# Kernel tuning notes

Hardware: AMD Instinct MI355X
Metric: run time of the kernel (lower is better)

Reference implementation:

```python
import jax, jax.numpy as jnp
import numpy as np

N, E, IN, H, B, R, ND, K, ER = 50000, 800000, 256, 256, 256, 8, 5000, 16, 20000
LAM = 0.7


def _gat(x, src, dst, W, a_src, a_dst, b):
    """Single-head PyG-style GATConv, add_self_loops=False."""
    h = x @ W                                   # [N,H]
    s = (h @ a_src)[src] + (h @ a_dst)[dst]     # [E]
    e = jax.nn.leaky_relu(s, 0.2)
    m = jax.ops.segment_max(e, dst, num_segments=N)
    m = jnp.where(jnp.isneginf(m), 0.0, m)
    p = jnp.exp(e - m[dst])
    z = jax.ops.segment_sum(p, dst, num_segments=N)
    alpha = p / (z[dst] + 1e-16)                # softmax over incoming edges
    out = jax.ops.segment_sum(alpha[:, None] * h[src], dst, num_segments=N)
    return out + b


def setup_inputs() -> dict:
    key = jax.random.key(0)
    ks = jax.random.split(key, 20)
    d = {}
    d['x'] = jax.random.normal(ks[0], (N, IN), dtype=jnp.float32)
    d['edge_index'] = jax.random.randint(ks[1], (2, E), 0, N)
    d['head_indices'] = jax.random.randint(ks[2], (B,), 0, N)
    d['rel_types'] = jax.random.randint(ks[3], (B,), 0, R)
    d['tail_indices'] = jax.random.randint(ks[4], (B,), 0, N)
    d['g2l'] = jax.random.randint(ks[5], (N,), 0, ND)
    d['rel_edge_src'] = jax.random.randint(ks[6], (3, ER), 0, ND)
    d['sim_neighbors'] = jax.random.randint(ks[7], (ND, K), 0, N)
    d['sim_weights'] = jax.random.uniform(ks[8], (ND, K), dtype=jnp.float32) / K
    sc1 = 1.0 / np.sqrt(IN)
    sc2 = 1.0 / np.sqrt(H)
    d['W1'] = jax.random.normal(ks[9], (IN, H), dtype=jnp.float32) * sc1
    d['a1_src'] = jax.random.normal(ks[10], (H,), dtype=jnp.float32) * sc2
    d['a1_dst'] = jax.random.normal(ks[11], (H,), dtype=jnp.float32) * sc2
    d['b1'] = jnp.zeros((H,), dtype=jnp.float32)
    d['W2'] = jax.random.normal(ks[12], (H, H), dtype=jnp.float32) * sc2
    d['a2_src'] = jax.random.normal(ks[13], (H,), dtype=jnp.float32) * sc2
    d['a2_dst'] = jax.random.normal(ks[14], (H,), dtype=jnp.float32) * sc2
    d['b2'] = jnp.zeros((H,), dtype=jnp.float32)
    d['rel_emb'] = jax.random.normal(ks[15], (R, H), dtype=jnp.float32) * sc2
    return d


def reference(x, edge_index, head_indices, rel_types, tail_indices, g2l,
              rel_edge_src, sim_neighbors, sim_weights,
              W1, a1_src, a1_dst, b1, W2, a2_src, a2_dst, b2, rel_emb):
    src, dst = edge_index[0], edge_index[1]
    # Encoder: GAT -> SiLU -> GAT
    h = _gat(x, src, dst, W1, a1_src, a1_dst, b1)
    h = jax.nn.silu(h)
    node_emb = _gat(h, src, dst, W2, a2_src, a2_dst, b2)  # [N,H]

    # Sequential per-triplet disease-embedding modification (rel 4/5/6)
    def step(emb, tr):
        hi, r = tr
        is_dis = (r >= 4) & (r <= 6)
        ridx = jnp.clip(r - 4, 0, 2)
        local = g2l[hi]
        deg = jnp.sum(rel_edge_src[ridx] == local).astype(emb.dtype)
        c = LAM * jnp.exp(-LAM * deg) + 0.2
        nb = sim_neighbors[local]           # [K]
        w = sim_weights[local]              # [K]
        vec = (w[:, None] * emb[nb]).sum(0)  # weighted neighbor mix
        new = c * vec + (1.0 - c) * emb[hi]
        row = jnp.where(is_dis, new, emb[hi])
        return emb.at[hi].set(row), None

    node_emb, _ = jax.lax.scan(step, node_emb, (head_indices, rel_types))

    # DistMult decode
    head = node_emb[head_indices]
    tail = node_emb[tail_indices]
    rel = rel_emb[rel_types]
    score = (head * rel * tail).sum(-1)
    return jax.nn.sigmoid(score)
```

## Files before the change

### kernel.cpp

```cpp
#include <hip/hip_runtime.h>
#include <cstdint>

#define N_NODES 50000
#define N_EDGES 800000
#define DIM     256
#define BSZ     256
#define ND_     5000
#define KNB     16
#define ER_     20000
#define LAM     0.7f

typedef unsigned int uint;
typedef unsigned short ushort;
typedef __attribute__((ext_vector_type(8))) short bf16x8;
typedef __attribute__((ext_vector_type(4))) float f32x4;

#define MTILES_PAD 3128
#define M_PAD      (MTILES_PAD*16)
#define NB_SCAN    ((N_NODES + 255) / 256)

__device__ __forceinline__ ushort f2bf(float f) {
    uint u = __float_as_uint(f);
    uint r = u + 0x7FFFu + ((u >> 16) & 1u);
    return (ushort)(r >> 16);
}
__device__ __forceinline__ float bflo(uint u) { return __uint_as_float(u << 16); }
__device__ __forceinline__ float bfhi(uint u) { return __uint_as_float(u & 0xffff0000u); }


__global__ __launch_bounds__(256)
void pack_a_kernel(const float* __restrict__ A, ushort* __restrict__ out, int M) {
    const int mt = blockIdx.x;
    const int t  = threadIdx.x;
    const int l  = t & 63;
    const int kt0 = (t >> 6) * 2;
    const int row = mt * 16 + (l & 15);
    const int lg  = l >> 4;
#pragma unroll
    for (int p = 0; p < 2; ++p) {
        int kt = kt0 + p;
        float4 v0 = make_float4(0.f, 0.f, 0.f, 0.f);
        float4 v1 = make_float4(0.f, 0.f, 0.f, 0.f);
        if (row < M) {
            v0 = *(const float4*)(A + (size_t)row * 256 + kt * 32 + lg * 4);
            v1 = *(const float4*)(A + (size_t)row * 256 + kt * 32 + lg * 4 + 16);
        }
        ushort us[8];
        us[0] = f2bf(v0.x); us[1] = f2bf(v0.y); us[2] = f2bf(v0.z); us[3] = f2bf(v0.w);
        us[4] = f2bf(v1.x); us[5] = f2bf(v1.y); us[6] = f2bf(v1.z); us[7] = f2bf(v1.w);
        ushort* dst = out + ((size_t)(mt * 8 + kt) * 64 + l) * 8;
        *(uint4*)dst = *(uint4*)us;
    }
}

__global__ __launch_bounds__(256)
void pack_a_bf16_kernel(const ushort* __restrict__ A, ushort* __restrict__ out, int M) {
    const int mt = blockIdx.x;
    const int t  = threadIdx.x;
    const int l  = t & 63;
    const int kt0 = (t >> 6) * 2;
    const int row = mt * 16 + (l & 15);
    const int lg  = l >> 4;
#pragma unroll
    for (int p = 0; p < 2; ++p) {
        int kt = kt0 + p;
        uint2 v0 = make_uint2(0u, 0u), v1 = make_uint2(0u, 0u);
        if (row < M) {
            v0 = *(const uint2*)(A + (size_t)row * 256 + kt * 32 + lg * 4);
            v1 = *(const uint2*)(A + (size_t)row * 256 + kt * 32 + 16 + lg * 4);
        }
        uint4 o; o.x = v0.x; o.y = v0.y; o.z = v1.x; o.w = v1.y;
        *(uint4*)(out + ((size_t)(mt * 8 + kt) * 64 + l) * 8) = o;
    }
}

__global__ __launch_bounds__(256)
void pack_b_kernel(const float* __restrict__ W, ushort* __restrict__ out) {
    const int nt = blockIdx.x;
    const int t  = threadIdx.x;
    const int l  = t & 63;
    const int kt0 = (t >> 6) * 2;
    const int n  = nt * 16 + (l & 15);
    const int lg = l >> 4;
#pragma unroll
    for (int p = 0; p < 2; ++p) {
        int kt = kt0 + p;
        ushort us[8];
#pragma unroll
        for (int j = 0; j < 8; ++j) {
            int kk = (j & 3) + lg * 4 + (j >> 2) * 16;
            us[j] = f2bf(W[(size_t)(kt * 32 + kk) * 256 + n]);
        }
        ushort* dst = out + ((size_t)(nt * 8 + kt) * 64 + l) * 8;
        *(uint4*)dst = *(uint4*)us;
    }
}

__global__ __launch_bounds__(256)
void gemm_bf16_kernel(const ushort* __restrict__ Ap, const ushort* __restrict__ Bp,
                      ushort* __restrict__ H,
                      const float* __restrict__ a_src, const float* __restrict__ a_dst,
                      float* __restrict__ hs, float* __restrict__ hd, int M) {
    __shared__ float sdS[4][64];
    __shared__ float sdD[4][64];
    const int t = threadIdx.x;
    const int w = t >> 6;
    const int l = t & 63;
    const int mt0 = blockIdx.x * 4;
    f32x4 acc[4][4];
#pragma unroll
    for (int i = 0; i < 4; ++i)
#pragma unroll
        for (int j = 0; j < 4; ++j) acc[i][j] = (f32x4){0.f, 0.f, 0.f, 0.f};

    for (int kt = 0; kt < 8; ++kt) {
        bf16x8 af[4], bfr[4];
#pragma unroll
        for (int mi = 0; mi < 4; ++mi)
            af[mi] = *(const bf16x8*)(Ap + ((size_t)((mt0 + mi) * 8 + kt) * 64 + l) * 8);
#pragma unroll
        for (int ni = 0; ni < 4; ++ni)
            bfr[ni] = *(const bf16x8*)(Bp + ((size_t)((w * 4 + ni) * 8 + kt) * 64 + l) * 8);
#pragma unroll
        for (int mi = 0; mi < 4; ++mi)
#pragma unroll
            for (int ni = 0; ni < 4; ++ni)
                acc[mi][ni] = __builtin_amdgcn_mfma_f32_16x16x32_bf16(
                    af[mi], bfr[ni], acc[mi][ni], 0, 0, 0);
    }
    const int rbase = (l >> 4) * 4;
    const int cb    = (l & 15);
    float asv[4], adv[4];
#pragma unroll
    for (int ni = 0; ni < 4; ++ni) {
        int col = (w * 4 + ni) * 16 + cb;
        asv[ni] = a_src[col];
        adv[ni] = a_dst[col];
    }
#pragma unroll
    for (int mi = 0; mi < 4; ++mi) {
#pragma unroll
        for (int r = 0; r < 4; ++r) {
            int row = (mt0 + mi) * 16 + rbase + r;
            float ps = 0.f, pd = 0.f;
#pragma unroll
            for (int ni = 0; ni < 4; ++ni) {
                float hv = acc[mi][ni][r];
                ps = fmaf(hv, asv[ni], ps);
                pd = fmaf(hv, adv[ni], pd);
                if (row < M) {
                    int col = (w * 4 + ni) * 16 + cb;
                    H[(size_t)row * 256 + col] = f2bf(hv);
                }
            }
#pragma unroll
            for (int o = 1; o < 16; o <<= 1) {
                ps += __shfl_xor(ps, o);
                pd += __shfl_xor(pd, o);
            }
            if (cb == 0) {
                sdS[w][mi * 16 + rbase + r] = ps;
                sdD[w][mi * 16 + rbase + r] = pd;
            }
        }
    }
    __syncthreads();
    if (t < 64) {
        int row = mt0 * 16 + t;
        if (row < M) {
            hs[row] = sdS[0][t] + sdS[1][t] + sdS[2][t] + sdS[3][t];
            hd[row] = sdD[0][t] + sdD[1][t] + sdD[2][t] + sdD[3][t];
        }
    }
}

__global__ __launch_bounds__(256)
void hist_kernel(const int* __restrict__ ei, int* __restrict__ deg) {
    int e = blockIdx.x * 256 + threadIdx.x;
    if (e < N_EDGES) atomicAdd(&deg[ei[N_EDGES + e]], 1);
}

__global__ __launch_bounds__(256)
void blockscan_kernel(const int* __restrict__ deg, int* __restrict__ off,
                      int* __restrict__ bsum) {
    __shared__ int s[256];
    const int b = blockIdx.x, t = threadIdx.x;
    const int idx = b * 256 + t;
    int v = (idx < N_NODES) ? deg[idx] : 0;
    s[t] = v;
    __syncthreads();
    for (int o = 1; o < 256; o <<= 1) {
        int x = (t >= o) ? s[t - o] : 0;
        __syncthreads();
        s[t] += x;
        __syncthreads();
    }
    if (idx < N_NODES) off[idx] = s[t] - v;
    if (t == 255) bsum[b] = s[255];
}

__global__ __launch_bounds__(256)
void scan_bsum_kernel(const int* __restrict__ bsum, int* __restrict__ bpre) {
    __shared__ int s[256];
    const int t = threadIdx.x;
    int v = (t < NB_SCAN) ? bsum[t] : 0;
    s[t] = v;
    __syncthreads();
    for (int o = 1; o < 256; o <<= 1) {
        int x = (t >= o) ? s[t - o] : 0;
        __syncthreads();
        s[t] += x;
        __syncthreads();
    }
    if (t < NB_SCAN) bpre[t] = s[t] - v;
    if (t == 255) bpre[NB_SCAN] = s[255];
}

__global__ __launch_bounds__(256)
void add_offsets_kernel(int* __restrict__ off, const int* __restrict__ bpre) {
    const int b = blockIdx.x, t = threadIdx.x;
    const int idx = b * 256 + t;
    if (idx < N_NODES) off[idx] += bpre[b];
    if (b == NB_SCAN - 1 && t == 255) off[N_NODES] = bpre[NB_SCAN];
}

__global__ __launch_bounds__(256)
void scatter_kernel(const int* __restrict__ ei, const int* __restrict__ off,
                    int* __restrict__ cnt, int* __restrict__ csr_src) {
    int e = blockIdx.x * 256 + threadIdx.x;
    if (e >= N_EDGES) return;
    int d = ei[N_EDGES + e];
    int pos = atomicAdd(&cnt[d], 1);
    csr_src[off[d] + pos] = ei[e];
}

__global__ __launch_bounds__(256)
void gat_aggr_kernel(const int* __restrict__ off, const int* __restrict__ csr_src,
                     const float* __restrict__ hs, const float* __restrict__ hd,
                     const ushort* __restrict__ hb, const float* __restrict__ bias,
                     float* __restrict__ out_f32, ushort* __restrict__ out_bf,
                     int do_silu) {
    const int d = blockIdx.x * 4 + (threadIdx.x >> 6);
    const int l = threadIdx.x & 63;
    if (d >= N_NODES) return;
    const int beg = off[d], end = off[d + 1];
    const float hdd = hd[d];

    float acc0 = 0.f, acc1 = 0.f, acc2 = 0.f, acc3 = 0.f;
    float zl = 0.f;
    const ushort* __restrict__ hcol = hb + l * 4;

    for (int c0 = beg; c0 < end; c0 += 64) {
        const int cn = min(end - c0, 64);
        int s = 0; float pexp = 0.f;
        if (l < cn) {
            s = csr_src[c0 + l];
            float v = hs[s] + hdd;
            v = (v >= 0.f) ? v : 0.2f * v;
            pexp = __expf(v);
        }
        zl += pexp;
        int j = 0;
        for (; j + 4 <= cn; j += 4) {
            int   s0 = __shfl(s, j),     s1 = __shfl(s, j + 1);
            int   s2 = __shfl(s, j + 2), s3 = __shfl(s, j + 3);
            float p0 = __shfl(pexp, j),     p1 = __shfl(pexp, j + 1);
            float p2 = __shfl(pexp, j + 2), p3 = __shfl(pexp, j + 3);
            uint2 r0 = *(const uint2*)(hcol + (size_t)s0 * DIM);
            uint2 r1 = *(const uint2*)(hcol + (size_t)s1 * DIM);
            uint2 r2 = *(const uint2*)(hcol + (size_t)s2 * DIM);
            uint2 r3 = *(const uint2*)(hcol + (size_t)s3 * DIM);
            acc0 = fmaf(p0, bflo(r0.x), acc0); acc1 = fmaf(p0, bfhi(r0.x), acc1);
            acc2 = fmaf(p0, bflo(r0.y), acc2); acc3 = fmaf(p0, bfhi(r0.y), acc3);
            acc0 = fmaf(p1, bflo(r1.x), acc0); acc1 = fmaf(p1, bfhi(r1.x), acc1);
            acc2 = fmaf(p1, bflo(r1.y), acc2); acc3 = fmaf(p1, bfhi(r1.y), acc3);
            acc0 = fmaf(p2, bflo(r2.x), acc0); acc1 = fmaf(p2, bfhi(r2.x), acc1);
            acc2 = fmaf(p2, bflo(r2.y), acc2); acc3 = fmaf(p2, bfhi(r2.y), acc3);
            acc0 = fmaf(p3, bflo(r3.x), acc0); acc1 = fmaf(p3, bfhi(r3.x), acc1);
            acc2 = fmaf(p3, bflo(r3.y), acc2); acc3 = fmaf(p3, bfhi(r3.y), acc3);
        }
        for (; j < cn; ++j) {
            int   sj = __shfl(s, j);
            float pj = __shfl(pexp, j);
            uint2 rv = *(const uint2*)(hcol + (size_t)sj * DIM);
            acc0 = fmaf(pj, bflo(rv.x), acc0); acc1 = fmaf(pj, bfhi(rv.x), acc1);
            acc2 = fmaf(pj, bflo(rv.y), acc2); acc3 = fmaf(pj, bfhi(rv.y), acc3);
        }
    }
    float z = zl;
#pragma unroll
    for (int o = 32; o; o >>= 1) z += __shfl_xor(z, o);
    const float inv = (end > beg) ? 1.f / (z + 1e-16f) : 0.f;
    float4 bb = *(const float4*)(bias + l * 4);
    float o0 = acc0 * inv + bb.x;
    float o1 = acc1 * inv + bb.y;
    float o2 = acc2 * inv + bb.z;
    float o3 = acc3 * inv + bb.w;
    if (do_silu) {
        o0 = o0 / (1.f + __expf(-o0));
        o1 = o1 / (1.f + __expf(-o1));
        o2 = o2 / (1.f + __expf(-o2));
        o3 = o3 / (1.f + __expf(-o3));
    }
    if (out_bf) {
        ushort us[4] = {f2bf(o0), f2bf(o1), f2bf(o2), f2bf(o3)};
        *(uint2*)(out_bf + (size_t)d * DIM + l * 4) = *(uint2*)us;
    } else {
        *(float4*)(out_f32 + (size_t)d * DIM + l * 4) = make_float4(o0, o1, o2, o3);
    }
}

__global__ __launch_bounds__(256)
void rel_hist_kernel(const int* __restrict__ res, int* __restrict__ rhist) {
    int i = blockIdx.x * 256 + threadIdx.x;
    if (i < 3 * ER_) atomicAdd(&rhist[(i / ER_) * ND_ + res[i]], 1);
}

__global__ __launch_bounds__(256)
void cvals_kernel(const int* __restrict__ rel, const int* __restrict__ head,
                  const int* __restrict__ g2l, const int* __restrict__ rhist,
                  float* __restrict__ cvals) {
    int b = threadIdx.x;
    int r = rel[b];
    float c = 0.f;
    if (r >= 4 && r <= 6) {
        int local = g2l[head[b]];
        int deg = rhist[(r - 4) * ND_ + local];
        c = LAM * __expf(-LAM * (float)deg) + 0.2f;
    }
    cvals[b] = c;
}

__global__ __launch_bounds__(256)
void prep_steps_kernel(const float* __restrict__ emb, const int* __restrict__ head,
                       const int* __restrict__ rel, const int* __restrict__ g2l,
                       const int* __restrict__ nbs, const float* __restrict__ wts,
                       float* __restrict__ vecpre, int* __restrict__ W,
                       int* __restrict__ flags) {
    int b = blockIdx.x;
    int t = threadIdx.x;
    int r = rel[b];
    int dis = (r >= 4 && r <= 6);
    if (t == 0) { flags[b] = 0; W[b] = dis ? head[b] : -1; }
    if (!dis) return;
    int local = g2l[head[b]];
    const int* __restrict__ nb = nbs + (size_t)local * KNB;
    const float* __restrict__ w = wts + (size_t)local * KNB;
    float v0 = 0.f, v1 = 0.f;
#pragma unroll
    for (int k = 0; k < KNB; k += 2) {
        v0 = fmaf(w[k],     emb[(size_t)nb[k] * DIM + t],     v0);
        v1 = fmaf(w[k + 1], emb[(size_t)nb[k + 1] * DIM + t], v1);
    }
    vecpre[(size_t)b * DIM + t] = v0 + v1;
}

__global__ __launch_bounds__(256)
void conflict_kernel(const int* __restrict__ W, const int* __restrict__ head,
                     const int* __restrict__ rel, const int* __restrict__ g2l,
                     const int* __restrict__ nbs, int* __restrict__ flags) {
    int b = blockIdx.x;
    int r = rel[b];
    if (r < 4 || r > 6) return;
    __shared__ int rd[KNB + 1];
    int t = threadIdx.x;
    if (t == 0) rd[KNB] = head[b];
    if (t < KNB) {
        int local = g2l[head[b]];
        rd[t] = nbs[(size_t)local * KNB + t];
    }
    __syncthreads();
    int w = (t != b) ? W[t] : -1;
    if (w >= 0) {
        bool hit = false;
#pragma unroll
        for (int k = 0; k <= KNB; ++k) hit |= (rd[k] == w);
        if (hit) { flags[b] = 1; flags[t] = 1; }
    }
}

__global__ __launch_bounds__(256)
void apply_par_kernel(float* __restrict__ emb, const int* __restrict__ head,
                      const int* __restrict__ rel, const float* __restrict__ cvals,
                      const float* __restrict__ vecpre, const int* __restrict__ flags) {
    int b = blockIdx.x;
    int r = rel[b];
    if (r < 4 || r > 6) return;
    if (flags[b]) return;
    int t = threadIdx.x;
    int hi = head[b];
    float c = cvals[b];
    size_t idx = (size_t)hi * DIM + t;
    emb[idx] = c * vecpre[(size_t)b * DIM + t] + (1.f - c) * emb[idx];
}

__global__ __launch_bounds__(256)
void apply_seq_kernel(float* __restrict__ emb, const int* __restrict__ head,
                      const int* __restrict__ rel, const int* __restrict__ g2l,
                      const int* __restrict__ nbs, const float* __restrict__ wts,
                      const float* __restrict__ cvals, const int* __restrict__ flags) {
    __shared__ int   snb[BSZ][KNB];
    __shared__ float sw[BSZ][KNB];
    __shared__ int   sh[BSZ];
    __shared__ float sc[BSZ];
    __shared__ int   sf[BSZ];
    const int t = threadIdx.x;
    int r = rel[t];
    int dis = (r >= 4 && r <= 6);
    int hi = head[t];
    sh[t] = hi;
    sc[t] = cvals[t];
    sf[t] = dis ? flags[t] : 0;
    if (dis) {
        int local = g2l[hi];
#pragma unroll
        for (int k = 0; k < KNB; ++k) {
            snb[t][k] = nbs[(size_t)local * KNB + k];
            sw[t][k]  = wts[(size_t)local * KNB + k];
        }
    }
    __syncthreads();
    for (int b = 0; b < BSZ; ++b) {
        if (sf[b]) {
            int hh = sh[b];
            float c = sc[b];
            float v0 = 0.f, v1 = 0.f;
#pragma unroll
            for (int k = 0; k < KNB; k += 2) {
                v0 = fmaf(sw[b][k],     emb[(size_t)snb[b][k] * DIM + t],     v0);
                v1 = fmaf(sw[b][k + 1], emb[(size_t)snb[b][k + 1] * DIM + t], v1);
            }
            size_t idx = (size_t)hh * DIM + t;
            emb[idx] = c * (v0 + v1) + (1.f - c) * emb[idx];
        }
    }
}

__global__ __launch_bounds__(256)
void decode_kernel(const float* __restrict__ emb, const int* __restrict__ head,
                   const int* __restrict__ rel, const int* __restrict__ tail,
                   const float* __restrict__ rel_emb, float* __restrict__ out) {
    int b = blockIdx.x, t = threadIdx.x;
    float v = emb[(size_t)head[b] * DIM + t] *
              rel_emb[(size_t)rel[b] * DIM + t] *
              emb[(size_t)tail[b] * DIM + t];
    __shared__ float red[4];
#pragma unroll
    for (int off = 32; off; off >>= 1) v += __shfl_down(v, off);
    int lane = t & 63, w = t >> 6;
    if (lane == 0) red[w] = v;
    __syncthreads();
    if (t == 0) {
        float s = red[0] + red[1] + red[2] + red[3];
        out[b] = 1.f / (1.f + expf(-s));
    }
}

extern "C" void kernel_launch(void* const* d_in, const int* in_sizes, int n_in,
                              void* d_out, int out_size, void* d_ws, size_t ws_size,
                              hipStream_t stream) {
    const float* x        = (const float*)d_in[0];
    const int*   ei       = (const int*)d_in[1];
    const int*   head     = (const int*)d_in[2];
    const int*   rel      = (const int*)d_in[3];
    const int*   tail     = (const int*)d_in[4];
    const int*   g2l      = (const int*)d_in[5];
    const int*   res      = (const int*)d_in[6];
    const int*   nbs      = (const int*)d_in[7];
    const float* wts      = (const float*)d_in[8];
    const float* W1       = (const float*)d_in[9];
    const float* a1s      = (const float*)d_in[10];
    const float* a1d      = (const float*)d_in[11];
    const float* b1       = (const float*)d_in[12];
    const float* W2       = (const float*)d_in[13];
    const float* a2s      = (const float*)d_in[14];
    const float* a2d      = (const float*)d_in[15];
    const float* b2       = (const float*)d_in[16];
    const float* rel_emb  = (const float*)d_in[17];
    float* out = (float*)d_out;

    char* ws = (char*)d_ws;
    size_t off_b = 0;
    auto alloc = [&](size_t bytes) {
        void* pp = ws + off_b;
        off_b += (bytes + 255) & ~(size_t)255;
        return pp;
    };
    float*  bufB    = (float*)alloc((size_t)N_NODES * DIM * 4);
    ushort* hb      = (ushort*)alloc((size_t)N_NODES * DIM * 2);
    ushort* h1b     = (ushort*)alloc((size_t)N_NODES * DIM * 2);
    float*  hs      = (float*)alloc((size_t)N_NODES * 4);
    float*  hd      = (float*)alloc((size_t)N_NODES * 4);
    int*    deg     = (int*)alloc((size_t)N_NODES * 4);
    int*    offs    = (int*)alloc((size_t)(N_NODES + 1) * 4);
    int*    cnt     = (int*)alloc((size_t)N_NODES * 4);
    int*    csr_src = (int*)alloc((size_t)N_EDGES * 4);
    int*    bsum    = (int*)alloc((size_t)NB_SCAN * 4);
    int*    bpre    = (int*)alloc((size_t)(NB_SCAN + 1) * 4);
    int*    rhist   = (int*)alloc((size_t)3 * ND_ * 4);
    float*  cvals   = (float*)alloc((size_t)BSZ * 4);
    float*  vecpre  = (float*)alloc((size_t)BSZ * DIM * 4);
    int*    Wrows   = (int*)alloc((size_t)BSZ * 4);
    int*    flags   = (int*)alloc((size_t)BSZ * 4);
    ushort* apack   = (ushort*)alloc((size_t)M_PAD * 256 * 2);
    ushort* wpack1  = (ushort*)alloc((size_t)256 * 256 * 2);
    ushort* wpack2  = (ushort*)alloc((size_t)256 * 256 * 2);

    const int edgeBlocks = (N_EDGES + 255) / 256;
    const int gemmBlocks = MTILES_PAD / 4;
    const int nodeBlocks4 = (N_NODES + 3) / 4;

    hipMemsetAsync(deg, 0, (size_t)N_NODES * 4, stream);
    hipMemsetAsync(cnt, 0, (size_t)N_NODES * 4, stream);
    hipMemsetAsync(rhist, 0, (size_t)3 * ND_ * 4, stream);
    hist_kernel<<<edgeBlocks, 256, 0, stream>>>(ei, deg);
    blockscan_kernel<<<NB_SCAN, 256, 0, stream>>>(deg, offs, bsum);
    scan_bsum_kernel<<<1, 256, 0, stream>>>(bsum, bpre);
    add_offsets_kernel<<<NB_SCAN, 256, 0, stream>>>(offs, bpre);
    scatter_kernel<<<edgeBlocks, 256, 0, stream>>>(ei, offs, cnt, csr_src);
    pack_b_kernel<<<16, 256, 0, stream>>>(W1, wpack1);
    pack_b_kernel<<<16, 256, 0, stream>>>(W2, wpack2);
    rel_hist_kernel<<<(3 * ER_ + 255) / 256, 256, 0, stream>>>(res, rhist);

    pack_a_kernel<<<MTILES_PAD, 256, 0, stream>>>(x, apack, N_NODES);
    gemm_bf16_kernel<<<gemmBlocks, 256, 0, stream>>>(apack, wpack1, hb, a1s, a1d,
                                                     hs, hd, N_NODES);
    gat_aggr_kernel<<<nodeBlocks4, 256, 0, stream>>>(offs, csr_src, hs, hd, hb, b1,
                                                     nullptr, h1b, 1);

    pack_a_bf16_kernel<<<MTILES_PAD, 256, 0, stream>>>(h1b, apack, N_NODES);
    gemm_bf16_kernel<<<gemmBlocks, 256, 0, stream>>>(apack, wpack2, hb, a2s, a2d,
                                                     hs, hd, N_NODES);
    gat_aggr_kernel<<<nodeBlocks4, 256, 0, stream>>>(offs, csr_src, hs, hd, hb, b2,
                                                     bufB, nullptr, 0);

    cvals_kernel<<<1, 256, 0, stream>>>(rel, head, g2l, rhist, cvals);
    prep_steps_kernel<<<BSZ, 256, 0, stream>>>(bufB, head, rel, g2l, nbs, wts,
                                               vecpre, Wrows, flags);
    conflict_kernel<<<BSZ, 256, 0, stream>>>(Wrows, head, rel, g2l, nbs, flags);
    apply_par_kernel<<<BSZ, 256, 0, stream>>>(bufB, head, rel, cvals, vecpre, flags);
    apply_seq_kernel<<<1, 256, 0, stream>>>(bufB, head, rel, g2l, nbs, wts, cvals, flags);
    decode_kernel<<<BSZ, 256, 0, stream>>>(bufB, head, rel, tail, rel_emb, out);
}
```

Baseline: 427.5 us.

## Fuse A-operand packing into GEMM, simplify CSR build, pipeline gathers, merge tail kernels

```diff
diff --git a/kernel.cpp b/kernel.cpp
--- a/kernel.cpp
+++ b/kernel.cpp
@@ -16,7 +16,6 @@
 typedef __attribute__((ext_vector_type(4))) float f32x4;
 
 #define MTILES_PAD 3128
-#define M_PAD      (MTILES_PAD*16)
 #define NB_SCAN    ((N_NODES + 255) / 256)
 
 __device__ __forceinline__ ushort f2bf(float f) {
@@ -28,50 +27,30 @@
 __device__ __forceinline__ float bfhi(uint u) { return __uint_as_float(u & 0xffff0000u); }
 
 
-__global__ __launch_bounds__(256)
-void pack_a_kernel(const float* __restrict__ A, ushort* __restrict__ out, int M) {
-    const int mt = blockIdx.x;
-    const int t  = threadIdx.x;
-    const int l  = t & 63;
-    const int kt0 = (t >> 6) * 2;
-    const int row = mt * 16 + (l & 15);
-    const int lg  = l >> 4;
-#pragma unroll
-    for (int p = 0; p < 2; ++p) {
-        int kt = kt0 + p;
-        float4 v0 = make_float4(0.f, 0.f, 0.f, 0.f);
-        float4 v1 = make_float4(0.f, 0.f, 0.f, 0.f);
-        if (row < M) {
-            v0 = *(const float4*)(A + (size_t)row * 256 + kt * 32 + lg * 4);
-            v1 = *(const float4*)(A + (size_t)row * 256 + kt * 32 + lg * 4 + 16);
-        }
-        ushort us[8];
-        us[0] = f2bf(v0.x); us[1] = f2bf(v0.y); us[2] = f2bf(v0.z); us[3] = f2bf(v0.w);
-        us[4] = f2bf(v1.x); us[5] = f2bf(v1.y); us[6] = f2bf(v1.z); us[7] = f2bf(v1.w);
-        ushort* dst = out + ((size_t)(mt * 8 + kt) * 64 + l) * 8;
-        *(uint4*)dst = *(uint4*)us;
-    }
-}
-
-__global__ __launch_bounds__(256)
-void pack_a_bf16_kernel(const ushort* __restrict__ A, ushort* __restrict__ out, int M) {
-    const int mt = blockIdx.x;
-    const int t  = threadIdx.x;
-    const int l  = t & 63;
-    const int kt0 = (t >> 6) * 2;
-    const int row = mt * 16 + (l & 15);
-    const int lg  = l >> 4;
-#pragma unroll
-    for (int p = 0; p < 2; ++p) {
-        int kt = kt0 + p;
-        uint2 v0 = make_uint2(0u, 0u), v1 = make_uint2(0u, 0u);
-        if (row < M) {
-            v0 = *(const uint2*)(A + (size_t)row * 256 + kt * 32 + lg * 4);
-            v1 = *(const uint2*)(A + (size_t)row * 256 + kt * 32 + 16 + lg * 4);
-        }
-        uint4 o; o.x = v0.x; o.y = v0.y; o.z = v1.x; o.w = v1.y;
-        *(uint4*)(out + ((size_t)(mt * 8 + kt) * 64 + l) * 8) = o;
-    }
+__device__ __forceinline__ bf16x8 make_af_f32(const float* __restrict__ A,
+                                              int row, int c0, int M) {
+    float4 v0 = make_float4(0.f, 0.f, 0.f, 0.f);
+    float4 v1 = make_float4(0.f, 0.f, 0.f, 0.f);
+    if (row < M) {
+        v0 = *(const float4*)(A + (size_t)row * 256 + c0);
+        v1 = *(const float4*)(A + (size_t)row * 256 + c0 + 16);
+    }
+    uint4 o;
+    o.x = (uint)f2bf(v0.x) | ((uint)f2bf(v0.y) << 16);
+    o.y = (uint)f2bf(v0.z) | ((uint)f2bf(v0.w) << 16);
+    o.z = (uint)f2bf(v1.x) | ((uint)f2bf(v1.y) << 16);
+    o.w = (uint)f2bf(v1.z) | ((uint)f2bf(v1.w) << 16);
+    return *(bf16x8*)&o;
+}
+__device__ __forceinline__ bf16x8 make_af_bf16(const ushort* __restrict__ A,
+                                               int row, int c0, int M) {
+    uint2 v0 = make_uint2(0u, 0u), v1 = make_uint2(0u, 0u);
+    if (row < M) {
+        v0 = *(const uint2*)(A + (size_t)row * 256 + c0);
+        v1 = *(const uint2*)(A + (size_t)row * 256 + c0 + 16);
+    }
+    uint4 o; o.x = v0.x; o.y = v0.y; o.z = v1.x; o.w = v1.y;
+    return *(bf16x8*)&o;
 }
 
 __global__ __launch_bounds__(256)
@@ -96,9 +75,10 @@
     }
 }
 
-__global__ __launch_bounds__(256)
-void gemm_bf16_kernel(const ushort* __restrict__ Ap, const ushort* __restrict__ Bp,
-                      ushort* __restrict__ H,
+template<int SRCF32>
+__global__ __launch_bounds__(256)
+void gemm_bf16_kernel(const float* __restrict__ Af, const ushort* __restrict__ Ab,
+                      const ushort* __restrict__ Bp, ushort* __restrict__ H,
                       const float* __restrict__ a_src, const float* __restrict__ a_dst,
                       float* __restrict__ hs, float* __restrict__ hd, int M) {
     __shared__ float sdS[4][64];
@@ -107,6 +87,8 @@
     const int w = t >> 6;
     const int l = t & 63;
     const int mt0 = blockIdx.x * 4;
+    const int cb  = (l & 15);
+    const int lg  = l >> 4;
     f32x4 acc[4][4];
 #pragma unroll
     for (int i = 0; i < 4; ++i)
@@ -115,9 +97,13 @@
 
     for (int kt = 0; kt < 8; ++kt) {
         bf16x8 af[4], bfr[4];
-#pragma unroll
-        for (int mi = 0; mi < 4; ++mi)
-            af[mi] = *(const bf16x8*)(Ap + ((size_t)((mt0 + mi) * 8 + kt) * 64 + l) * 8);
+        const int c0 = kt * 32 + lg * 4;
+#pragma unroll
+        for (int mi = 0; mi < 4; ++mi) {
+            int row = (mt0 + mi) * 16 + cb;
+            af[mi] = SRCF32 ? make_af_f32(Af, row, c0, M)
+                            : make_af_bf16(Ab, row, c0, M);
+        }
 #pragma unroll
         for (int ni = 0; ni < 4; ++ni)
             bfr[ni] = *(const bf16x8*)(Bp + ((size_t)((w * 4 + ni) * 8 + kt) * 64 + l) * 8);
@@ -129,7 +115,6 @@
                     af[mi], bfr[ni], acc[mi][ni], 0, 0, 0);
     }
     const int rbase = (l >> 4) * 4;
-    const int cb    = (l & 15);
     float asv[4], adv[4];
 #pragma unroll
     for (int ni = 0; ni < 4; ++ni) {
@@ -213,7 +198,6 @@
         __syncthreads();
     }
     if (t < NB_SCAN) bpre[t] = s[t] - v;
-    if (t == 255) bpre[NB_SCAN] = s[255];
 }
 
 __global__ __launch_bounds__(256)
@@ -221,17 +205,16 @@
     const int b = blockIdx.x, t = threadIdx.x;
     const int idx = b * 256 + t;
     if (idx < N_NODES) off[idx] += bpre[b];
-    if (b == NB_SCAN - 1 && t == 255) off[N_NODES] = bpre[NB_SCAN];
-}
-
-__global__ __launch_bounds__(256)
-void scatter_kernel(const int* __restrict__ ei, const int* __restrict__ off,
-                    int* __restrict__ cnt, int* __restrict__ csr_src) {
+}
+
+__global__ __launch_bounds__(256)
+void scatter_kernel(const int* __restrict__ ei, int* __restrict__ off,
+                    int* __restrict__ csr_src) {
     int e = blockIdx.x * 256 + threadIdx.x;
     if (e >= N_EDGES) return;
     int d = ei[N_EDGES + e];
-    int pos = atomicAdd(&cnt[d], 1);
-    csr_src[off[d] + pos] = ei[e];
+    int pos = atomicAdd(&off[d], 1);
+    csr_src[pos] = ei[e];
 }
 
 __global__ __launch_bounds__(256)
@@ -243,7 +226,8 @@
     const int d = blockIdx.x * 4 + (threadIdx.x >> 6);
     const int l = threadIdx.x & 63;
     if (d >= N_NODES) return;
-    const int beg = off[d], end = off[d + 1];
+    const int beg = d ? off[d - 1] : 0;
+    const int end = off[d];
     const float hdd = hd[d];
 
     float acc0 = 0.f, acc1 = 0.f, acc2 = 0.f, acc3 = 0.f;
@@ -260,16 +244,35 @@
             pexp = __expf(v);
         }
         zl += pexp;
+        const int nb4 = cn & ~3;
         int j = 0;
-        for (; j + 4 <= cn; j += 4) {
-            int   s0 = __shfl(s, j),     s1 = __shfl(s, j + 1);
-            int   s2 = __shfl(s, j + 2), s3 = __shfl(s, j + 3);
-            float p0 = __shfl(pexp, j),     p1 = __shfl(pexp, j + 1);
-            float p2 = __shfl(pexp, j + 2), p3 = __shfl(pexp, j + 3);
+        if (nb4) {
+            int s0 = __shfl(s, 0), s1 = __shfl(s, 1), s2 = __shfl(s, 2), s3 = __shfl(s, 3);
             uint2 r0 = *(const uint2*)(hcol + (size_t)s0 * DIM);
             uint2 r1 = *(const uint2*)(hcol + (size_t)s1 * DIM);
             uint2 r2 = *(const uint2*)(hcol + (size_t)s2 * DIM);
             uint2 r3 = *(const uint2*)(hcol + (size_t)s3 * DIM);
+            for (j = 4; j < nb4; j += 4) {
+                int sn0 = __shfl(s, j),     sn1 = __shfl(s, j + 1);
+                int sn2 = __shfl(s, j + 2), sn3 = __shfl(s, j + 3);
+                uint2 q0 = *(const uint2*)(hcol + (size_t)sn0 * DIM);
+                uint2 q1 = *(const uint2*)(hcol + (size_t)sn1 * DIM);
+                uint2 q2 = *(const uint2*)(hcol + (size_t)sn2 * DIM);
+                uint2 q3 = *(const uint2*)(hcol + (size_t)sn3 * DIM);
+                float p0 = __shfl(pexp, j - 4), p1 = __shfl(pexp, j - 3);
+                float p2 = __shfl(pexp, j - 2), p3 = __shfl(pexp, j - 1);
+                acc0 = fmaf(p0, bflo(r0.x), acc0); acc1 = fmaf(p0, bfhi(r0.x), acc1);
+                acc2 = fmaf(p0, bflo(r0.y), acc2); acc3 = fmaf(p0, bfhi(r0.y), acc3);
+                acc0 = fmaf(p1, bflo(r1.x), acc0); acc1 = fmaf(p1, bfhi(r1.x), acc1);
+                acc2 = fmaf(p1, bflo(r1.y), acc2); acc3 = fmaf(p1, bfhi(r1.y), acc3);
+                acc0 = fmaf(p2, bflo(r2.x), acc0); acc1 = fmaf(p2, bfhi(r2.x), acc1);
+                acc2 = fmaf(p2, bflo(r2.y), acc2); acc3 = fmaf(p2, bfhi(r2.y), acc3);
+                acc0 = fmaf(p3, bflo(r3.x), acc0); acc1 = fmaf(p3, bfhi(r3.x), acc1);
+                acc2 = fmaf(p3, bflo(r3.y), acc2); acc3 = fmaf(p3, bfhi(r3.y), acc3);
+                r0 = q0; r1 = q1; r2 = q2; r3 = q3;
+            }
+            float p0 = __shfl(pexp, j - 4), p1 = __shfl(pexp, j - 3);
+            float p2 = __shfl(pexp, j - 2), p3 = __shfl(pexp, j - 1);
             acc0 = fmaf(p0, bflo(r0.x), acc0); acc1 = fmaf(p0, bfhi(r0.x), acc1);
             acc2 = fmaf(p0, bflo(r0.y), acc2); acc3 = fmaf(p0, bfhi(r0.y), acc3);
             acc0 = fmaf(p1, bflo(r1.x), acc0); acc1 = fmaf(p1, bfhi(r1.x), acc1);
@@ -317,60 +320,19 @@
 }
 
 __global__ __launch_bounds__(256)
-void cvals_kernel(const int* __restrict__ rel, const int* __restrict__ head,
-                  const int* __restrict__ g2l, const int* __restrict__ rhist,
-                  float* __restrict__ cvals) {
-    int b = threadIdx.x;
-    int r = rel[b];
-    float c = 0.f;
-    if (r >= 4 && r <= 6) {
-        int local = g2l[head[b]];
-        int deg = rhist[(r - 4) * ND_ + local];
-        c = LAM * __expf(-LAM * (float)deg) + 0.2f;
-    }
-    cvals[b] = c;
-}
-
-__global__ __launch_bounds__(256)
-void prep_steps_kernel(const float* __restrict__ emb, const int* __restrict__ head,
-                       const int* __restrict__ rel, const int* __restrict__ g2l,
-                       const int* __restrict__ nbs, const float* __restrict__ wts,
-                       float* __restrict__ vecpre, int* __restrict__ W,
-                       int* __restrict__ flags) {
+void conflict_kernel(const int* __restrict__ head, const int* __restrict__ rel,
+                     const int* __restrict__ g2l, const int* __restrict__ nbs,
+                     int* __restrict__ flags) {
     int b = blockIdx.x;
-    int t = threadIdx.x;
-    int r = rel[b];
-    int dis = (r >= 4 && r <= 6);
-    if (t == 0) { flags[b] = 0; W[b] = dis ? head[b] : -1; }
-    if (!dis) return;
-    int local = g2l[head[b]];
-    const int* __restrict__ nb = nbs + (size_t)local * KNB;
-    const float* __restrict__ w = wts + (size_t)local * KNB;
-    float v0 = 0.f, v1 = 0.f;
-#pragma unroll
-    for (int k = 0; k < KNB; k += 2) {
-        v0 = fmaf(w[k],     emb[(size_t)nb[k] * DIM + t],     v0);
-        v1 = fmaf(w[k + 1], emb[(size_t)nb[k + 1] * DIM + t], v1);
-    }
-    vecpre[(size_t)b * DIM + t] = v0 + v1;
-}
-
-__global__ __launch_bounds__(256)
-void conflict_kernel(const int* __restrict__ W, const int* __restrict__ head,
-                     const int* __restrict__ rel, const int* __restrict__ g2l,
-                     const int* __restrict__ nbs, int* __restrict__ flags) {
-    int b = blockIdx.x;
-    int r = rel[b];
-    if (r < 4 || r > 6) return;
+    int rb = rel[b];
+    if (rb < 4 || rb > 6) return;
     __shared__ int rd[KNB + 1];
     int t = threadIdx.x;
     if (t == 0) rd[KNB] = head[b];
-    if (t < KNB) {
-        int local = g2l[head[b]];
-        rd[t] = nbs[(size_t)local * KNB + t];
-    }
+    if (t < KNB) rd[t] = nbs[(size_t)g2l[head[b]] * KNB + t];
     __syncthreads();
-    int w = (t != b) ? W[t] : -1;
+    int rt = rel[t];
+    int w = (t != b && rt >= 4 && rt <= 6) ? head[t] : -1;
     if (w >= 0) {
         bool hit = false;
 #pragma unroll
@@ -380,39 +342,46 @@
 }
 
 __global__ __launch_bounds__(256)
-void apply_par_kernel(float* __restrict__ emb, const int* __restrict__ head,
-                      const int* __restrict__ rel, const float* __restrict__ cvals,
-                      const float* __restrict__ vecpre, const int* __restrict__ flags) {
-    int b = blockIdx.x;
-    int r = rel[b];
-    if (r < 4 || r > 6) return;
-    if (flags[b]) return;
-    int t = threadIdx.x;
-    int hi = head[b];
-    float c = cvals[b];
-    size_t idx = (size_t)hi * DIM + t;
-    emb[idx] = c * vecpre[(size_t)b * DIM + t] + (1.f - c) * emb[idx];
-}
-
-__global__ __launch_bounds__(256)
-void apply_seq_kernel(float* __restrict__ emb, const int* __restrict__ head,
-                      const int* __restrict__ rel, const int* __restrict__ g2l,
-                      const int* __restrict__ nbs, const float* __restrict__ wts,
-                      const float* __restrict__ cvals, const int* __restrict__ flags) {
+void apply_kernel(float* __restrict__ emb, const int* __restrict__ head,
+                  const int* __restrict__ rel, const int* __restrict__ g2l,
+                  const int* __restrict__ nbs, const float* __restrict__ wts,
+                  const int* __restrict__ rhist, const int* __restrict__ flags) {
+    const int t = threadIdx.x;
+    if (blockIdx.x < BSZ) {
+        int b = blockIdx.x;
+        int r = rel[b];
+        if (r < 4 || r > 6) return;
+        if (flags[b]) return;
+        int hi = head[b];
+        int local = g2l[hi];
+        int dg = rhist[(r - 4) * ND_ + local];
+        float c = LAM * __expf(-LAM * (float)dg) + 0.2f;
+        const int* __restrict__ nb = nbs + (size_t)local * KNB;
+        const float* __restrict__ w = wts + (size_t)local * KNB;
+        float v0 = 0.f, v1 = 0.f;
+#pragma unroll
+        for (int k = 0; k < KNB; k += 2) {
+            v0 = fmaf(w[k],     emb[(size_t)nb[k] * DIM + t],     v0);
+            v1 = fmaf(w[k + 1], emb[(size_t)nb[k + 1] * DIM + t], v1);
+        }
+        size_t idx = (size_t)hi * DIM + t;
+        emb[idx] = c * (v0 + v1) + (1.f - c) * emb[idx];
+        return;
+    }
     __shared__ int   snb[BSZ][KNB];
     __shared__ float sw[BSZ][KNB];
     __shared__ int   sh[BSZ];
     __shared__ float sc[BSZ];
     __shared__ int   sf[BSZ];
-    const int t = threadIdx.x;
     int r = rel[t];
     int dis = (r >= 4 && r <= 6);
     int hi = head[t];
     sh[t] = hi;
-    sc[t] = cvals[t];
     sf[t] = dis ? flags[t] : 0;
     if (dis) {
         int local = g2l[hi];
+        int dg = rhist[(r - 4) * ND_ + local];
+        sc[t] = LAM * __expf(-LAM * (float)dg) + 0.2f;
 #pragma unroll
         for (int k = 0; k < KNB; ++k) {
             snb[t][k] = nbs[(size_t)local * KNB + k];
@@ -491,18 +460,15 @@
     ushort* h1b     = (ushort*)alloc((size_t)N_NODES * DIM * 2);
     float*  hs      = (float*)alloc((size_t)N_NODES * 4);
     float*  hd      = (float*)alloc((size_t)N_NODES * 4);
+    size_t z0 = off_b;
     int*    deg     = (int*)alloc((size_t)N_NODES * 4);
+    int*    rhist   = (int*)alloc((size_t)3 * ND_ * 4);
+    int*    flags   = (int*)alloc((size_t)BSZ * 4);
+    size_t z1 = off_b;
     int*    offs    = (int*)alloc((size_t)(N_NODES + 1) * 4);
-    int*    cnt     = (int*)alloc((size_t)N_NODES * 4);
     int*    csr_src = (int*)alloc((size_t)N_EDGES * 4);
     int*    bsum    = (int*)alloc((size_t)NB_SCAN * 4);
-    int*    bpre    = (int*)alloc((size_t)(NB_SCAN + 1) * 4);
-    int*    rhist   = (int*)alloc((size_t)3 * ND_ * 4);
-    float*  cvals   = (float*)alloc((size_t)BSZ * 4);
-    float*  vecpre  = (float*)alloc((size_t)BSZ * DIM * 4);
-    int*    Wrows   = (int*)alloc((size_t)BSZ * 4);
-    int*    flags   = (int*)alloc((size_t)BSZ * 4);
-    ushort* apack   = (ushort*)alloc((size_t)M_PAD * 256 * 2);
+    int*    bpre    = (int*)alloc((size_t)NB_SCAN * 4);
     ushort* wpack1  = (ushort*)alloc((size_t)256 * 256 * 2);
     ushort* wpack2  = (ushort*)alloc((size_t)256 * 256 * 2);
 
@@ -510,35 +476,28 @@
     const int gemmBlocks = MTILES_PAD / 4;
     const int nodeBlocks4 = (N_NODES + 3) / 4;
 
-    hipMemsetAsync(deg, 0, (size_t)N_NODES * 4, stream);
-    hipMemsetAsync(cnt, 0, (size_t)N_NODES * 4, stream);
-    hipMemsetAsync(rhist, 0, (size_t)3 * ND_ * 4, stream);
+    hipMemsetAsync(ws + z0, 0, z1 - z0, stream);
     hist_kernel<<<edgeBlocks, 256, 0, stream>>>(ei, deg);
     blockscan_kernel<<<NB_SCAN, 256, 0, stream>>>(deg, offs, bsum);
     scan_bsum_kernel<<<1, 256, 0, stream>>>(bsum, bpre);
     add_offsets_kernel<<<NB_SCAN, 256, 0, stream>>>(offs, bpre);
-    scatter_kernel<<<edgeBlocks, 256, 0, stream>>>(ei, offs, cnt, csr_src);
+    scatter_kernel<<<edgeBlocks, 256, 0, stream>>>(ei, offs, csr_src);
     pack_b_kernel<<<16, 256, 0, stream>>>(W1, wpack1);
     pack_b_kernel<<<16, 256, 0, stream>>>(W2, wpack2);
     rel_hist_kernel<<<(3 * ER_ + 255) / 256, 256, 0, stream>>>(res, rhist);
 
-    pack_a_kernel<<<MTILES_PAD, 256, 0, stream>>>(x, apack, N_NODES);
-    gemm_bf16_kernel<<<gemmBlocks, 256, 0, stream>>>(apack, wpack1, hb, a1s, a1d,
-                                                     hs, hd, N_NODES);
+    gemm_bf16_kernel<1><<<gemmBlocks, 256, 0, stream>>>(x, nullptr, wpack1, hb,
+                                                        a1s, a1d, hs, hd, N_NODES);
     gat_aggr_kernel<<<nodeBlocks4, 256, 0, stream>>>(offs, csr_src, hs, hd, hb, b1,
                                                      nullptr, h1b, 1);
 
-    pack_a_bf16_kernel<<<MTILES_PAD, 256, 0, stream>>>(h1b, apack, N_NODES);
-    gemm_bf16_kernel<<<gemmBlocks, 256, 0, stream>>>(apack, wpack2, hb, a2s, a2d,
-                                                     hs, hd, N_NODES);
+    gemm_bf16_kernel<0><<<gemmBlocks, 256, 0, stream>>>(nullptr, h1b, wpack2, hb,
+                                                        a2s, a2d, hs, hd, N_NODES);
     gat_aggr_kernel<<<nodeBlocks4, 256, 0, stream>>>(offs, csr_src, hs, hd, hb, b2,
                                                      bufB, nullptr, 0);
 
-    cvals_kernel<<<1, 256, 0, stream>>>(rel, head, g2l, rhist, cvals);
-    prep_steps_kernel<<<BSZ, 256, 0, stream>>>(bufB, head, rel, g2l, nbs, wts,
-                                               vecpre, Wrows, flags);
-    conflict_kernel<<<BSZ, 256, 0, stream>>>(Wrows, head, rel, g2l, nbs, flags);
-    apply_par_kernel<<<BSZ, 256, 0, stream>>>(bufB, head, rel, cvals, vecpre, flags);
-    apply_seq_kernel<<<1, 256, 0, stream>>>(bufB, head, rel, g2l, nbs, wts, cvals, flags);
+    conflict_kernel<<<BSZ, 256, 0, stream>>>(head, rel, g2l, nbs, flags);
+    apply_kernel<<<BSZ + 1, 256, 0, stream>>>(bufB, head, rel, g2l, nbs, wts,
+                                              rhist, flags);
     decode_kernel<<<BSZ, 256, 0, stream>>>(bufB, head, rel, tail, rel_emb, out);
 }
```

Measured after the change: 439.6 us. 1.03x slower.
